# Performance work log

Hardware: AMD Instinct MI355X
Metric: run time of the kernel (lower is better)

Reference implementation:

```python
import jax, jax.numpy as jnp
import numpy as np

NUM_HEADS = 16

def setup_inputs() -> dict:
    key = jax.random.key(0)
    ks = jax.random.split(key, 5)
    B, S, H = 16, 1025, 1024
    std = 0.02
    return {
        "hidden_states": jax.random.normal(ks[0], (B, S, H), jnp.float32),
        "w_qkv": jax.random.normal(ks[1], (3 * H, H), jnp.float32) * std,
        "b_qkv": jax.random.normal(ks[2], (3 * H,), jnp.float32) * std,
        "w_dense": jax.random.normal(ks[3], (H, H), jnp.float32) * std,
        "b_dense": jax.random.normal(ks[4], (H,), jnp.float32) * std,
    }

def reference(hidden_states, w_qkv, b_qkv, w_dense, b_dense):
    B, S, H = hidden_states.shape
    nh = NUM_HEADS
    hd = H // nh
    scale = hd ** -0.5
    # fused QKV projection: [B,S,3H]
    mixed = jnp.einsum('bsh,oh->bso', hidden_states, w_qkv) + b_qkv
    # reshape per torch: (B,S,nh,3,hd) -> permute(3,0,2,1,4)
    mixed = mixed.reshape(B, S, nh, 3, hd).transpose(3, 0, 2, 1, 4)
    q, k, v = mixed[0], mixed[1], mixed[2]          # each [B,nh,S,hd]
    scores = jnp.einsum('bhqd,bhkd->bhqk', q, k) * scale
    probs = jax.nn.softmax(scores, axis=-1)          # [B,nh,S,S]
    ctx = jnp.einsum('bhqk,bhkd->bhqd', probs, v)    # [B,nh,S,hd]
    ctx = ctx.transpose(0, 2, 1, 3).reshape(B, S, H)
    out = jnp.einsum('bsh,oh->bso', ctx, w_dense) + b_dense
    return out
```

## Files before the change

### kernel.cpp

```cpp
#include <hip/hip_runtime.h>
#include <math.h>

typedef float f32x4 __attribute__((ext_vector_type(4)));
typedef __bf16 bf16x8 __attribute__((ext_vector_type(8)));
typedef unsigned int u32;
typedef u32 u32x4 __attribute__((ext_vector_type(4)));

#define AS1 __attribute__((address_space(1)))
#define AS3 __attribute__((address_space(3)))

static __device__ __forceinline__ void gload16(const void* g, void* l) {
    __builtin_amdgcn_global_load_lds((const AS1 u32*)g, (AS3 u32*)l, 16, 0, 0);
}
static __device__ __forceinline__ f32x4 mfma16(bf16x8 a, bf16x8 b, f32x4 c) {
    return __builtin_amdgcn_mfma_f32_16x16x32_bf16(a, b, c, 0, 0, 0);
}
static __device__ __forceinline__ float exp2fast(float x) {
    return __builtin_amdgcn_exp2f(x);
}

__global__ __launch_bounds__(256)
void convert_kernel(const float* __restrict__ in, __bf16* __restrict__ out)
{
    const size_t i = ((size_t)blockIdx.x * 256 + threadIdx.x) * 8;
    f32x4 a = *(const f32x4*)(in + i);
    f32x4 b = *(const f32x4*)(in + i + 4);
    bf16x8 o;
    #pragma unroll
    for (int j = 0; j < 4; ++j) { o[j] = (__bf16)a[j]; o[j + 4] = (__bf16)b[j]; }
    *(bf16x8*)(out + i) = o;
}

__global__ __launch_bounds__(512, 2)
void gemm_qkv256(const __bf16* __restrict__ A, const __bf16* __restrict__ Bw,
                 const float* __restrict__ bias,
                 __bf16* __restrict__ q_out, __bf16* __restrict__ k_out,
                 __bf16* __restrict__ v_out)
{
    constexpr int M = 16400;
    constexpr int K = 1024;
    constexpr int NKT = 16;
    constexpr int NWG = 12 * 65;

    __shared__ __align__(16) __bf16 ldsA[2][256 * 64];
    __shared__ __align__(16) __bf16 ldsB[2][256 * 64];

    const int tid  = threadIdx.x;
    const int lane = tid & 63;
    const int wv   = tid >> 6;
    const int wr   = wv >> 2;
    const int wc   = wv & 3;
    const int fr   = lane & 15, fq = lane >> 4;

    int flat = blockIdx.x;
    {
        constexpr int Q = NWG / 8, R = NWG % 8;
        const int x = flat % 8, j = flat / 8;
        flat = (x < R ? x * (Q + 1) : R * (Q + 1) + (x - R) * Q) + j;
    }
    const int bx = flat / 65, by = flat % 65;
    const int m0 = by * 256, n0 = bx * 256;

    const __bf16* aSrc[2][2]; int aDst[2][2];
    #pragma unroll
    for (int g = 0; g < 2; ++g)
        #pragma unroll
        for (int l = 0; l < 2; ++l) {
            const int s    = l * 512 + tid;
            const int sr   = s >> 3, gran = s & 7;
            const int row  = (sr & 63) + g * 64 + ((sr >> 6) << 7);
            const int c    = gran ^ (row & 7);
            int m = m0 + row; if (m > M - 1) m = M - 1;
            aSrc[g][l] = A + (size_t)m * K + c * 8;
            aDst[g][l] = (row * 8 + gran) * 8;
        }
    const __bf16* bSrc[2][2]; int bDst[2][2];
    #pragma unroll
    for (int n = 0; n < 2; ++n)
        #pragma unroll
        for (int l = 0; l < 2; ++l) {
            const int q   = l * 2 + (tid >> 8);
            const int p   = tid & 255;
            const int row = q * 64 + n * 32 + (p >> 3);
            const int g   = p & 7;
            const int c   = g ^ (row & 7);
            bSrc[n][l] = Bw + (size_t)(n0 + row) * K + c * 8;
            bDst[n][l] = (row * 8 + g) * 8;
        }

#define STAGE_A(g, nb, ko) { \
    gload16(aSrc[g][0] + (ko), &ldsA[nb][aDst[g][0]]); \
    gload16(aSrc[g][1] + (ko), &ldsA[nb][aDst[g][1]]); }
#define STAGE_B(n, nb, ko) { \
    gload16(bSrc[n][0] + (ko), &ldsB[nb][bDst[n][0]]); \
    gload16(bSrc[n][1] + (ko), &ldsB[nb][bDst[n][1]]); }

    f32x4 acc[8][4];
    #pragma unroll
    for (int i = 0; i < 8; ++i)
        #pragma unroll
        for (int j = 0; j < 4; ++j)
            acc[i][j] = f32x4{0.f, 0.f, 0.f, 0.f};

    const int slot0 = ((0 + fq) ^ (fr & 7)) * 8;
    const int slot1 = ((4 + fq) ^ (fr & 7)) * 8;
    const int arow  = wr * 128 + fr;
    const int brow  = wc * 64 + fr;

    STAGE_A(0, 0, 0); STAGE_B(0, 0, 0); STAGE_B(1, 0, 0); STAGE_A(1, 0, 0);
    STAGE_A(0, 1, 64); STAGE_A(1, 1, 64);

    for (int t = 0; t < NKT; ++t) {
        const int cur = t & 1, nxt = cur ^ 1;
        const int ko1 = (t + 1 < NKT ? t + 1 : NKT - 1) * 64;
        const int ko2 = (t + 2 < NKT ? t + 2 : NKT - 1) * 64;
        bf16x8 a[4][2], b[2][2];

        STAGE_B(0, nxt, ko1);
        asm volatile("s_waitcnt vmcnt(8)" ::: "memory");
        __builtin_amdgcn_s_barrier();
        #pragma unroll
        for (int i = 0; i < 4; ++i) {
            a[i][0] = *(const bf16x8*)&ldsA[cur][(arow + i * 16) * 64 + slot0];
            a[i][1] = *(const bf16x8*)&ldsA[cur][(arow + i * 16) * 64 + slot1];
        }
        #pragma unroll
        for (int j = 0; j < 2; ++j) {
            b[j][0] = *(const bf16x8*)&ldsB[cur][(brow + j * 16) * 64 + slot0];
            b[j][1] = *(const bf16x8*)&ldsB[cur][(brow + j * 16) * 64 + slot1];
        }
        __builtin_amdgcn_s_setprio(1);
        #pragma unroll
        for (int ks = 0; ks < 2; ++ks)
            #pragma unroll
            for (int i = 0; i < 4; ++i)
                #pragma unroll
                for (int j = 0; j < 2; ++j)
                    acc[i][j] = mfma16(a[i][ks], b[j][ks], acc[i][j]);
        __builtin_amdgcn_s_setprio(0);

        STAGE_B(1, nxt, ko1);
        STAGE_A(0, cur, ko2);
        asm volatile("s_waitcnt vmcnt(10)" ::: "memory");
        __builtin_amdgcn_s_barrier();
        #pragma unroll
        for (int j = 0; j < 2; ++j) {
            b[j][0] = *(const bf16x8*)&ldsB[cur][(brow + 32 + j * 16) * 64 + slot0];
            b[j][1] = *(const bf16x8*)&ldsB[cur][(brow + 32 + j * 16) * 64 + slot1];
        }
        __builtin_amdgcn_s_setprio(1);
        #pragma unroll
        for (int ks = 0; ks < 2; ++ks)
            #pragma unroll
            for (int i = 0; i < 4; ++i)
                #pragma unroll
                for (int j = 0; j < 2; ++j)
                    acc[i][2 + j] = mfma16(a[i][ks], b[j][ks], acc[i][2 + j]);
        __builtin_amdgcn_s_setprio(0);

        #pragma unroll
        for (int i = 0; i < 4; ++i) {
            a[i][0] = *(const bf16x8*)&ldsA[cur][(arow + 64 + i * 16) * 64 + slot0];
            a[i][1] = *(const bf16x8*)&ldsA[cur][(arow + 64 + i * 16) * 64 + slot1];
        }
        #pragma unroll
        for (int j = 0; j < 2; ++j) {
            b[j][0] = *(const bf16x8*)&ldsB[cur][(brow + j * 16) * 64 + slot0];
            b[j][1] = *(const bf16x8*)&ldsB[cur][(brow + j * 16) * 64 + slot1];
        }
        __builtin_amdgcn_s_setprio(1);
        #pragma unroll
        for (int ks = 0; ks < 2; ++ks)
            #pragma unroll
            for (int i = 0; i < 4; ++i)
                #pragma unroll
                for (int j = 0; j < 2; ++j)
                    acc[4 + i][j] = mfma16(a[i][ks], b[j][ks], acc[4 + i][j]);
        __builtin_amdgcn_s_setprio(0);

        __builtin_amdgcn_s_barrier();
        STAGE_A(1, cur, ko2);
        #pragma unroll
        for (int j = 0; j < 2; ++j) {
            b[j][0] = *(const bf16x8*)&ldsB[cur][(brow + 32 + j * 16) * 64 + slot0];
            b[j][1] = *(const bf16x8*)&ldsB[cur][(brow + 32 + j * 16) * 64 + slot1];
        }
        __builtin_amdgcn_s_setprio(1);
        #pragma unroll
        for (int ks = 0; ks < 2; ++ks)
            #pragma unroll
            for (int i = 0; i < 4; ++i)
                #pragma unroll
                for (int j = 0; j < 2; ++j)
                    acc[4 + i][2 + j] = mfma16(a[i][ks], b[j][ks], acc[4 + i][2 + j]);
        __builtin_amdgcn_s_setprio(0);
    }
    asm volatile("s_waitcnt vmcnt(0)" ::: "memory");

    #pragma unroll
    for (int ni = 0; ni < 4; ++ni) {
        const int col = n0 + wc * 64 + ni * 16 + fr;
        const float bv = bias[col];
        const int head = col / 192;
        const int tsel = (col >> 6) % 3;
        const int d    = col & 63;
        __bf16* dst = (tsel == 0) ? q_out : (tsel == 1 ? k_out : v_out);
        const float scale = (tsel == 0) ? 0.18033688011112042f : 1.0f;
        #pragma unroll
        for (int mi = 0; mi < 8; ++mi) {
            #pragma unroll
            for (int j = 0; j < 4; ++j) {
                const int m = m0 + wr * 128 + mi * 16 + fq * 4 + j;
                if (m < M) {
                    const int bb = m / 1025;
                    const int ss = m - bb * 1025;
                    dst[(((size_t)(bb * 16 + head)) * 1025 + ss) * 64 + d] =
                        (__bf16)((acc[mi][ni][j] + bv) * scale);
                }
            }
        }
    }
#undef STAGE_A
#undef STAGE_B
}

__global__ __launch_bounds__(256)
void gemm_dense128(const __bf16* __restrict__ A, const __bf16* __restrict__ Bw,
                   const float* __restrict__ bias, float* __restrict__ f_out)
{
    constexpr int M = 16400;
    constexpr int K = 1024;

    __shared__ __align__(16) __bf16 As[128 * 64];
    __shared__ __align__(16) __bf16 Bs[128 * 64];

    const int tid  = threadIdx.x;
    const int lane = tid & 63;
    const int wv   = tid >> 6;
    const int wr   = wv >> 1, wc = wv & 1;
    const int fr   = lane & 15, fq = lane >> 4;
    const int m0   = blockIdx.y * 128;
    const int n0   = blockIdx.x * 128;

    const __bf16* aptr[4];
    const __bf16* bptr[4];
    int loff[4];
    #pragma unroll
    for (int qd = 0; qd < 4; ++qd) {
        const int s  = qd * 256 + tid;
        const int r  = s >> 3;
        const int c  = (s & 7) ^ (r & 7);
        loff[qd] = s * 8;
        int ar = m0 + r; if (ar > M - 1) ar = M - 1;
        aptr[qd] = A  + (size_t)ar * K + c * 8;
        bptr[qd] = Bw + (size_t)(n0 + r) * K + c * 8;
    }

    f32x4 acc[4][4];
    #pragma unroll
    for (int i = 0; i < 4; ++i)
        #pragma unroll
        for (int j = 0; j < 4; ++j)
            acc[i][j] = f32x4{0.f, 0.f, 0.f, 0.f};

    for (int kt = 0; kt < K / 64; ++kt) {
        const int kof = kt * 64;
        #pragma unroll
        for (int qd = 0; qd < 4; ++qd) {
            gload16(aptr[qd] + kof, &As[loff[qd]]);
            gload16(bptr[qd] + kof, &Bs[loff[qd]]);
        }
        __syncthreads();

        #pragma unroll
        for (int ks = 0; ks < 2; ++ks) {
            bf16x8 a[4], b[4];
            #pragma unroll
            for (int i = 0; i < 4; ++i) {
                const int ra = wr * 64 + i * 16 + fr;
                const int rb = wc * 64 + i * 16 + fr;
                const int cg = ((ks * 4 + fq) ^ (fr & 7)) * 8;
                a[i] = *(const bf16x8*)&As[ra * 64 + cg];
                b[i] = *(const bf16x8*)&Bs[rb * 64 + cg];
            }
            #pragma unroll
            for (int i = 0; i < 4; ++i)
                #pragma unroll
                for (int j = 0; j < 4; ++j)
                    acc[i][j] = mfma16(a[i], b[j], acc[i][j]);
        }
        __syncthreads();
    }

    #pragma unroll
    for (int ni = 0; ni < 4; ++ni) {
        const int col = n0 + wc * 64 + ni * 16 + fr;
        const float bv = bias[col];
        #pragma unroll
        for (int mi = 0; mi < 4; ++mi) {
            #pragma unroll
            for (int j = 0; j < 4; ++j) {
                const int m = m0 + wr * 64 + mi * 16 + fq * 4 + j;
                if (m < M) f_out[(size_t)m * 1024 + col] = acc[mi][ni][j] + bv;
            }
        }
    }
}

__global__ __launch_bounds__(256)
void transpose_v(const __bf16* __restrict__ vb, __bf16* __restrict__ vt)
{
    constexpr int S = 1025, S2 = 1088;
    const int bh = blockIdx.y;
    const int s0 = blockIdx.x * 64;
    const int sr = threadIdx.x >> 2, sq = threadIdx.x & 3;
    int srow = s0 + sr; if (srow > S - 1) srow = S - 1;
    const __bf16* src = vb + ((size_t)bh * S + srow) * 64 + sq * 16;
    bf16x8 v0 = *(const bf16x8*)src;
    bf16x8 v1 = *(const bf16x8*)(src + 8);
    __bf16* dst = vt + (size_t)bh * 64 * S2 + s0 + sr;
    #pragma unroll
    for (int i = 0; i < 8; ++i) {
        dst[(size_t)(sq * 16 + i) * S2]     = v0[i];
        dst[(size_t)(sq * 16 + 8 + i) * S2] = v1[i];
    }
}

__global__ __launch_bounds__(256)
void attn_kernel(const __bf16* __restrict__ qb, const __bf16* __restrict__ kb,
                 const __bf16* __restrict__ vtb, __bf16* __restrict__ ctxb)
{
    constexpr int S = 1025, S2 = 1088;
    const int tid  = threadIdx.x;
    const int lane = tid & 63;
    const int w    = tid >> 6;
    const int fr   = lane & 15, fq = lane >> 4;
    const int bh   = blockIdx.y;
    const int q0   = blockIdx.x * 64;
    const int bb   = bh >> 4, hh = bh & 15;

    const __bf16* qp = qb  + (size_t)bh * S * 64;
    const __bf16* kp = kb  + (size_t)bh * S * 64;
    const __bf16* vp = vtb + (size_t)bh * 64 * S2;

    __shared__ __align__(16) __bf16 Ks[64 * 64];
    __shared__ __align__(16) __bf16 Vs[64 * 64];
    __shared__ u32 Ps[4][16 * 33];

    const int s0i = tid, s1i = tid + 256;
    const int r0 = s0i >> 3, g0 = (s0i & 7) ^ (r0 & 7);
    const int r1 = s1i >> 3, g1 = (s1i & 7) ^ (r1 & 7);
    const __bf16* vsrc0 = vp + (size_t)r0 * S2 + g0 * 8;
    const __bf16* vsrc1 = vp + (size_t)r1 * S2 + g1 * 8;

    int qrow = q0 + w * 16 + fr; if (qrow > S - 1) qrow = S - 1;
    const bf16x8 qa0 = *(const bf16x8*)(qp + (size_t)qrow * 64 + fq * 8);
    const bf16x8 qa1 = *(const bf16x8*)(qp + (size_t)qrow * 64 + 32 + fq * 8);

    f32x4 ctx[4];
    #pragma unroll
    for (int di = 0; di < 4; ++di) ctx[di] = f32x4{0.f, 0.f, 0.f, 0.f};
    float mrow = -1e30f;
    float lrow = 0.f;

    u32* psrow_w = &Ps[w][fr * 33];

    for (int kt = 0; kt < 17; ++kt) {
        const int kv0 = kt * 64;
        {
            int kr0 = kv0 + r0; if (kr0 > S - 1) kr0 = S - 1;
            int kr1 = kv0 + r1; if (kr1 > S - 1) kr1 = S - 1;
            gload16(kp + (size_t)kr0 * 64 + g0 * 8, &Ks[s0i * 8]);
            gload16(kp + (size_t)kr1 * 64 + g1 * 8, &Ks[s1i * 8]);
            gload16(vsrc0 + kv0, &Vs[s0i * 8]);
            gload16(vsrc1 + kv0, &Vs[s1i * 8]);
        }
        __syncthreads();

        f32x4 sc[4];
        #pragma unroll
        for (int ni = 0; ni < 4; ++ni) {
            const int row = ni * 16 + fr;
            bf16x8 kf0 = *(const bf16x8*)&Ks[row * 64 + ((fq    ) ^ (row & 7)) * 8];
            bf16x8 kf1 = *(const bf16x8*)&Ks[row * 64 + ((fq + 4) ^ (row & 7)) * 8];
            f32x4 z = f32x4{0.f, 0.f, 0.f, 0.f};
            z = mfma16(kf0, qa0, z);
            sc[ni] = mfma16(kf1, qa1, z);
        }
        if (kv0 + 64 > S) {
            #pragma unroll
            for (int ni = 0; ni < 4; ++ni)
                #pragma unroll
                for (int j = 0; j < 4; ++j)
                    if (kv0 + ni * 16 + fq * 4 + j >= S) sc[ni][j] = -1e30f;
        }

        float mt = sc[0][0];
        #pragma unroll
        for (int ni = 0; ni < 4; ++ni)
            #pragma unroll
            for (int j = 0; j < 4; ++j) mt = fmaxf(mt, sc[ni][j]);
        mt = fmaxf(mt, __shfl_xor(mt, 16, 64));
        mt = fmaxf(mt, __shfl_xor(mt, 32, 64));

        if (__any(mt > mrow + 8.0f)) {
            const float mnew = fmaxf(mrow, mt);
            const float alpha = exp2fast(mrow - mnew);
            mrow = mnew;
            lrow *= alpha;
            float a[4];
            #pragma unroll
            for (int j = 0; j < 4; ++j) a[j] = __shfl(alpha, fq * 4 + j, 64);
            #pragma unroll
            for (int di = 0; di < 4; ++di) {
                ctx[di][0] *= a[0]; ctx[di][1] *= a[1];
                ctx[di][2] *= a[2]; ctx[di][3] *= a[3];
            }
        }

        float p[4][4];
        float s = 0.f;
        #pragma unroll
        for (int ni = 0; ni < 4; ++ni)
            #pragma unroll
            for (int j = 0; j < 4; ++j) {
                p[ni][j] = exp2fast(sc[ni][j] - mrow);
                s += p[ni][j];
            }
        s += __shfl_xor(s, 16, 64);
        s += __shfl_xor(s, 32, 64);
        lrow += s;

        #pragma unroll
        for (int ni = 0; ni < 4; ++ni) {
            #pragma unroll
            for (int h = 0; h < 2; ++h) {
                unsigned short lo = __builtin_bit_cast(unsigned short, (__bf16)p[ni][2 * h]);
                unsigned short hi = __builtin_bit_cast(unsigned short, (__bf16)p[ni][2 * h + 1]);
                psrow_w[fq * 8 + ni * 2 + h] = (u32)lo | ((u32)hi << 16);
            }
        }
        u32x4 pav[2];
        #pragma unroll
        for (int ks = 0; ks < 2; ++ks)
            #pragma unroll
            for (int t = 0; t < 4; ++t) {
                const int slot = (2 * (fq & 1) + (t >> 1)) * 8
                               + (2 * ks + (fq >> 1)) * 2 + (t & 1);
                pav[ks][t] = psrow_w[slot];
            }

        #pragma unroll
        for (int ks = 0; ks < 2; ++ks) {
            const bf16x8 pa = __builtin_bit_cast(bf16x8, pav[ks]);
            #pragma unroll
            for (int di = 0; di < 4; ++di) {
                const int row = di * 16 + fr;
                bf16x8 vf = *(const bf16x8*)&Vs[row * 64 + ((ks * 4 + fq) ^ (row & 7)) * 8];
                ctx[di] = mfma16(pa, vf, ctx[di]);
            }
        }
        __syncthreads();
    }

    float linv[4];
    #pragma unroll
    for (int j = 0; j < 4; ++j) linv[j] = 1.0f / __shfl(lrow, fq * 4 + j, 64);
    #pragma unroll
    for (int di = 0; di < 4; ++di) {
        #pragma unroll
        for (int j = 0; j < 4; ++j) {
            const int qg = q0 + w * 16 + fq * 4 + j;
            if (qg < S) {
                ctxb[((size_t)bb * 1025 + qg) * 1024 + hh * 64 + di * 16 + fr] =
                    (__bf16)(ctx[di][j] * linv[j]);
            }
        }
    }
}

extern "C" void kernel_launch(void* const* d_in, const int* in_sizes, int n_in,
                              void* d_out, int out_size, void* d_ws, size_t ws_size,
                              hipStream_t stream)
{
    const float* hs      = (const float*)d_in[0];
    const float* w_qkv   = (const float*)d_in[1];
    const float* b_qkv   = (const float*)d_in[2];
    const float* w_dense = (const float*)d_in[3];
    const float* b_dense = (const float*)d_in[4];

    const size_t nHS = (size_t)16 * 1025 * 1024;
    const size_t nWQ = (size_t)3072 * 1024;
    const size_t nWD = (size_t)1024 * 1024;

    __bf16* hsb     = (__bf16*)d_ws;
    __bf16* wqkvb   = hsb + nHS;
    __bf16* wdenseb = wqkvb + nWQ;
    __bf16* qb      = wdenseb + nWD;
    __bf16* kb      = qb + nHS;
    __bf16* vb      = kb + nHS;
    __bf16* ctxb    = vb + nHS;
    __bf16* vtb     = ctxb + nHS;

    dim3 blk(256);
    convert_kernel<<<dim3((unsigned)(nHS / 2048)), blk, 0, stream>>>(hs, hsb);
    convert_kernel<<<dim3((unsigned)(nWQ / 2048)), blk, 0, stream>>>(w_qkv, wqkvb);
    convert_kernel<<<dim3((unsigned)(nWD / 2048)), blk, 0, stream>>>(w_dense, wdenseb);

    gemm_qkv256<<<dim3(12 * 65), dim3(512), 0, stream>>>(
        hsb, wqkvb, b_qkv, qb, kb, vb);

    transpose_v<<<dim3(17, 256), blk, 0, stream>>>(vb, vtb);

    attn_kernel<<<dim3(17, 256), blk, 0, stream>>>(qb, kb, vtb, ctxb);

    gemm_dense128<<<dim3(8, 129), blk, 0, stream>>>(
        ctxb, wdenseb, b_dense, (float*)d_out);
}
```

Measured before the change: 464.6 us.

## Restructure QKV GEMM prefetch pipeline and add XCD-aware tile remapping

The QKV GEMM drops its two-tile-ahead A prefetch for a one-tile-ahead schedule. Each of the four sub-steps now stages one quarter of the next tile into the other buffer, followed by a fixed vmcnt(6) wait and explicit barriers, and the quadrant order changes. The GEMM tile order becomes row-major over N, and the attention and dense GEMM grids are flattened to 1D with a remap that gives each of the 8 XCDs a contiguous chunk of tiles. The aim is better L2 locality per XCD and simpler waitcnt and barrier handling. In exchange there are more barriers per K-step and less prefetch distance.

```diff
diff --git a/kernel.cpp b/kernel.cpp
--- a/kernel.cpp
+++ b/kernel.cpp
@@ -52,13 +52,13 @@
     const int wc   = wv & 3;
     const int fr   = lane & 15, fq = lane >> 4;
 
-    int flat = blockIdx.x;
+    int tile;
     {
         constexpr int Q = NWG / 8, R = NWG % 8;
-        const int x = flat % 8, j = flat / 8;
-        flat = (x < R ? x * (Q + 1) : R * (Q + 1) + (x - R) * Q) + j;
-    }
-    const int bx = flat / 65, by = flat % 65;
+        const int x = blockIdx.x & 7, j = blockIdx.x >> 3;
+        tile = (x < R ? x * (Q + 1) : R * (Q + 1) + (x - R) * Q) + j;
+    }
+    const int by = tile / 12, bx = tile % 12;
     const int m0 = by * 256, n0 = bx * 256;
 
     const __bf16* aSrc[2][2]; int aDst[2][2];
@@ -94,6 +94,8 @@
 #define STAGE_B(n, nb, ko) { \
     gload16(bSrc[n][0] + (ko), &ldsB[nb][bDst[n][0]]); \
     gload16(bSrc[n][1] + (ko), &ldsB[nb][bDst[n][1]]); }
+#define WAIT6_BAR  asm volatile("s_waitcnt vmcnt(6)\ns_barrier" ::: "memory")
+#define BAR        asm volatile("s_barrier" ::: "memory")
 
     f32x4 acc[8][4];
     #pragma unroll
@@ -108,17 +110,14 @@
     const int brow  = wc * 64 + fr;
 
     STAGE_A(0, 0, 0); STAGE_B(0, 0, 0); STAGE_B(1, 0, 0); STAGE_A(1, 0, 0);
-    STAGE_A(0, 1, 64); STAGE_A(1, 1, 64);
-
+
+    bf16x8 a[4][2], b[2][2];
     for (int t = 0; t < NKT; ++t) {
         const int cur = t & 1, nxt = cur ^ 1;
-        const int ko1 = (t + 1 < NKT ? t + 1 : NKT - 1) * 64;
-        const int ko2 = (t + 2 < NKT ? t + 2 : NKT - 1) * 64;
-        bf16x8 a[4][2], b[2][2];
-
-        STAGE_B(0, nxt, ko1);
-        asm volatile("s_waitcnt vmcnt(8)" ::: "memory");
-        __builtin_amdgcn_s_barrier();
+        const int ko  = (t + 1 < NKT ? t + 1 : NKT - 1) * 64;
+
+        STAGE_A(0, nxt, ko);
+        WAIT6_BAR;
         #pragma unroll
         for (int i = 0; i < 4; ++i) {
             a[i][0] = *(const bf16x8*)&ldsA[cur][(arow + i * 16) * 64 + slot0];
@@ -138,11 +137,10 @@
                 for (int j = 0; j < 2; ++j)
                     acc[i][j] = mfma16(a[i][ks], b[j][ks], acc[i][j]);
         __builtin_amdgcn_s_setprio(0);
-
-        STAGE_B(1, nxt, ko1);
-        STAGE_A(0, cur, ko2);
-        asm volatile("s_waitcnt vmcnt(10)" ::: "memory");
-        __builtin_amdgcn_s_barrier();
+        BAR;
+
+        STAGE_B(0, nxt, ko);
+        WAIT6_BAR;
         #pragma unroll
         for (int j = 0; j < 2; ++j) {
             b[j][0] = *(const bf16x8*)&ldsB[cur][(brow + 32 + j * 16) * 64 + slot0];
@@ -157,12 +155,28 @@
                 for (int j = 0; j < 2; ++j)
                     acc[i][2 + j] = mfma16(a[i][ks], b[j][ks], acc[i][2 + j]);
         __builtin_amdgcn_s_setprio(0);
-
+        BAR;
+
+        STAGE_B(1, nxt, ko);
+        WAIT6_BAR;
         #pragma unroll
         for (int i = 0; i < 4; ++i) {
             a[i][0] = *(const bf16x8*)&ldsA[cur][(arow + 64 + i * 16) * 64 + slot0];
             a[i][1] = *(const bf16x8*)&ldsA[cur][(arow + 64 + i * 16) * 64 + slot1];
         }
+        __builtin_amdgcn_s_setprio(1);
+        #pragma unroll
+        for (int ks = 0; ks < 2; ++ks)
+            #pragma unroll
+            for (int i = 0; i < 4; ++i)
+                #pragma unroll
+                for (int j = 0; j < 2; ++j)
+                    acc[4 + i][2 + j] = mfma16(a[i][ks], b[j][ks], acc[4 + i][2 + j]);
+        __builtin_amdgcn_s_setprio(0);
+        BAR;
+
+        STAGE_A(1, nxt, ko);
+        BAR;
         #pragma unroll
         for (int j = 0; j < 2; ++j) {
             b[j][0] = *(const bf16x8*)&ldsB[cur][(brow + j * 16) * 64 + slot0];
@@ -177,23 +191,7 @@
                 for (int j = 0; j < 2; ++j)
                     acc[4 + i][j] = mfma16(a[i][ks], b[j][ks], acc[4 + i][j]);
         __builtin_amdgcn_s_setprio(0);
-
-        __builtin_amdgcn_s_barrier();
-        STAGE_A(1, cur, ko2);
-        #pragma unroll
-        for (int j = 0; j < 2; ++j) {
-            b[j][0] = *(const bf16x8*)&ldsB[cur][(brow + 32 + j * 16) * 64 + slot0];
-            b[j][1] = *(const bf16x8*)&ldsB[cur][(brow + 32 + j * 16) * 64 + slot1];
-        }
-        __builtin_amdgcn_s_setprio(1);
-        #pragma unroll
-        for (int ks = 0; ks < 2; ++ks)
-            #pragma unroll
-            for (int i = 0; i < 4; ++i)
-                #pragma unroll
-                for (int j = 0; j < 2; ++j)
-                    acc[4 + i][2 + j] = mfma16(a[i][ks], b[j][ks], acc[4 + i][2 + j]);
-        __builtin_amdgcn_s_setprio(0);
+        BAR;
     }
     asm volatile("s_waitcnt vmcnt(0)" ::: "memory");
 
@@ -222,6 +220,8 @@
     }
 #undef STAGE_A
 #undef STAGE_B
+#undef WAIT6_BAR
+#undef BAR
 }
 
 __global__ __launch_bounds__(256)
@@ -239,8 +239,11 @@
     const int wv   = tid >> 6;
     const int wr   = wv >> 1, wc = wv & 1;
     const int fr   = lane & 15, fq = lane >> 4;
-    const int m0   = blockIdx.y * 128;
-    const int n0   = blockIdx.x * 128;
+
+    const int xx = blockIdx.x & 7, jj = blockIdx.x >> 3;
+    const int tile = xx * 129 + jj;
+    const int m0 = (tile >> 3) * 128;
+    const int n0 = (tile & 7) * 128;
 
     const __bf16* aptr[4];
     const __bf16* bptr[4];
@@ -335,9 +338,12 @@
     const int lane = tid & 63;
     const int w    = tid >> 6;
     const int fr   = lane & 15, fq = lane >> 4;
-    const int bh   = blockIdx.y;
-    const int q0   = blockIdx.x * 64;
-    const int bb   = bh >> 4, hh = bh & 15;
+
+    const int xx = blockIdx.x & 7, jj = blockIdx.x >> 3;
+    const int tile = xx * 544 + jj;
+    const int bh = tile / 17;
+    const int q0 = (tile % 17) * 64;
+    const int bb = bh >> 4, hh = bh & 15;
 
     const __bf16* qp = qb  + (size_t)bh * S * 64;
     const __bf16* kp = kb  + (size_t)bh * S * 64;
@@ -408,13 +414,13 @@
             const float alpha = exp2fast(mrow - mnew);
             mrow = mnew;
             lrow *= alpha;
-            float a[4];
-            #pragma unroll
-            for (int j = 0; j < 4; ++j) a[j] = __shfl(alpha, fq * 4 + j, 64);
+            float av[4];
+            #pragma unroll
+            for (int j = 0; j < 4; ++j) av[j] = __shfl(alpha, fq * 4 + j, 64);
             #pragma unroll
             for (int di = 0; di < 4; ++di) {
-                ctx[di][0] *= a[0]; ctx[di][1] *= a[1];
-                ctx[di][2] *= a[2]; ctx[di][3] *= a[3];
+                ctx[di][0] *= av[0]; ctx[di][1] *= av[1];
+                ctx[di][2] *= av[2]; ctx[di][3] *= av[3];
             }
         }
 
@@ -512,8 +518,8 @@
 
     transpose_v<<<dim3(17, 256), blk, 0, stream>>>(vb, vtb);
 
-    attn_kernel<<<dim3(17, 256), blk, 0, stream>>>(qb, kb, vtb, ctxb);
-
-    gemm_dense128<<<dim3(8, 129), blk, 0, stream>>>(
+    attn_kernel<<<dim3(8 * 544), blk, 0, stream>>>(qb, kb, vtb, ctxb);
+
+    gemm_dense128<<<dim3(8 * 129), blk, 0, stream>>>(
         ctxb, wdenseb, b_dense, (float*)d_out);
 }
```

Measured after the change: 487.0 us. +4.8%, slower.
